# Kernel optimization log

Hardware: AMD Instinct MI355X
Metric: run time of the kernel (lower is better)

Reference implementation:

```python
import jax, jax.numpy as jnp
import numpy as np

N, E, F = 50000, 400000, 128
H0, C0 = 1, 128   # layer 0: heads=1, out=128 (concat=False -> mean over heads)
H1, C1 = 4, 64    # layer 1: heads=4, out=64
EPS_BN = 1e-5
NEG_SLOPE = 0.2


def setup_inputs() -> dict:
    key = jax.random.key(0)
    ks = jax.random.split(key, 12)

    def w(k, shape, fan_in):
        return jax.random.normal(k, shape, jnp.float32) / np.float32(np.sqrt(fan_in))

    return {
        "emb": jax.random.normal(ks[0], (N, F), jnp.float32),
        "edge_weight": jax.random.uniform(ks[1], (E,), jnp.float32),
        # GATv2Conv layer 0 params (lin_l, lin_r, lin_edge, att, out bias)
        "Wl0": w(ks[2], (F, H0 * C0), F), "bl0": jnp.zeros((H0 * C0,), jnp.float32),
        "Wr0": w(ks[3], (F, H0 * C0), F), "br0": jnp.zeros((H0 * C0,), jnp.float32),
        "We0": w(ks[4], (1, H0 * C0), 1), "att0": w(ks[5], (H0, C0), C0),
        "b0": jnp.zeros((C0,), jnp.float32),
        "g0": jnp.ones((C0,), jnp.float32), "be0": jnp.zeros((C0,), jnp.float32),
        # GATv2Conv layer 1 params
        "Wl1": w(ks[6], (C0, H1 * C1), C0), "bl1": jnp.zeros((H1 * C1,), jnp.float32),
        "Wr1": w(ks[7], (C0, H1 * C1), C0), "br1": jnp.zeros((H1 * C1,), jnp.float32),
        "We1": w(ks[8], (1, H1 * C1), 1), "att1": w(ks[9], (H1, C1), C1),
        "b1": jnp.zeros((C1,), jnp.float32),
        "g1": jnp.ones((C1,), jnp.float32), "be1": jnp.zeros((C1,), jnp.float32),
        "edge_index": jax.random.randint(ks[10], (2, E), 0, N, jnp.int32),
    }


def gatv2(x, src, dst, ea, Wl, bl, Wr, br, We, att, b, H, C):
    """PyG GATv2Conv, edge_dim=1, concat=False (mean over heads), eval dropout."""
    n = x.shape[0]
    xl = (x @ Wl + bl).reshape(n, H, C)
    xr = (x @ Wr + br).reshape(n, H, C)
    ef = (ea[:, None] @ We).reshape(-1, H, C)           # [Et,H,C] edge embedding
    m = jax.nn.leaky_relu(xl[src] + xr[dst] + ef, NEG_SLOPE)  # [Et,H,C]
    alpha = jnp.einsum('ehc,hc->eh', m, att)            # attention logits
    amax = jax.ops.segment_max(alpha, dst, num_segments=n)
    ex = jnp.exp(alpha - amax[dst])
    den = jax.ops.segment_sum(ex, dst, num_segments=n)
    a = ex / (den[dst] + 1e-16)                          # segment softmax (PyG eps)
    out = jax.ops.segment_sum(a[:, :, None] * xl[src], dst, num_segments=n)
    return out.mean(axis=1) + b                          # concat=False -> head mean


def batchnorm(x, g, be):
    mu = x.mean(0)
    v = x.var(0)  # biased variance, as torch BN uses for normalization
    return g * (x - mu) * jax.lax.rsqrt(v + EPS_BN) + be


def _forward(emb, edge_weight, Wl0, bl0, Wr0, br0, We0, att0, b0, g0, be0,
             Wl1, bl1, Wr1, br1, We1, att1, b1, g1, be1, edge_index):
    loop = jnp.arange(N, dtype=edge_index.dtype)
    src = jnp.concatenate([edge_index[0], loop])
    dst = jnp.concatenate([edge_index[1], loop])
    # add_self_loops with fill_value='mean' for edge_attr
    ea = jnp.concatenate([edge_weight, jnp.full((N,), edge_weight.mean(), edge_weight.dtype)])
    # NOTE: zip(layer_stack, batchnorm_stack) truncates -> only first 2 of 3 GAT
    # layers execute, each followed by BN + ELU (+ identity dropout, p=0).
    h = gatv2(emb, src, dst, ea, Wl0, bl0, Wr0, br0, We0, att0, b0, H0, C0)
    h = jax.nn.elu(batchnorm(h, g0, be0))
    h = gatv2(h, src, dst, ea, Wl1, bl1, Wr1, br1, We1, att1, b1, H1, C1)
    h = jax.nn.elu(batchnorm(h, g1, be1))
    return h


def reference(emb, edge_weight, Wl0, bl0, Wr0, br0, We0, att0, b0, g0, be0,
              Wl1, bl1, Wr1, br1, We1, att1, b1, g1, be1, edge_index):
    return _forward(emb, edge_weight, Wl0, bl0, Wr0, br0, We0, att0, b0, g0, be0,
                    Wl1, bl1, Wr1, br1, We1, att1, b1, g1, be1, edge_index)
```

## Files before the change

### kernel.cpp

```cpp
#include <hip/hip_runtime.h>
#include <cstdint>
#include <cstddef>
#include <type_traits>

using f32x4 = __attribute__((ext_vector_type(4))) float;
using s16x8 = __attribute__((ext_vector_type(8))) short;

__device__ __forceinline__ ushort f2bf(float x) {
    uint32_t u = __builtin_bit_cast(uint32_t, x);
    u += 0x7fffu + ((u >> 16) & 1u);
    return (ushort)(u >> 16);
}
__device__ __forceinline__ float bflo(uint32_t u) { return __builtin_bit_cast(float, u << 16); }
__device__ __forceinline__ float bfhi(uint32_t u) { return __builtin_bit_cast(float, u & 0xffff0000u); }

__device__ __forceinline__ void dec8(uint4 g, float* x) {
    x[0] = bflo(g.x); x[1] = bfhi(g.x); x[2] = bflo(g.y); x[3] = bfhi(g.y);
    x[4] = bflo(g.z); x[5] = bfhi(g.z); x[6] = bflo(g.w); x[7] = bfhi(g.w);
}

#define GLOAD_LDS16(g, l)                                                                  \
    __builtin_amdgcn_global_load_lds((const __attribute__((address_space(1))) void*)(g),  \
                                     (__attribute__((address_space(3))) void*)(l), 16, 0, 0)

__global__ __launch_bounds__(256) void degree_ew_kernel(const int* __restrict__ ei,
                                                        const float* __restrict__ ew,
                                                        int* __restrict__ deg,
                                                        float* __restrict__ partials,
                                                        int E, int N) {
    __shared__ float red[256];
    int t = threadIdx.x;
    int e = blockIdx.x * 256 + t;
    float s = (e < E) ? ew[e] : 0.f;
    red[t] = s; __syncthreads();
    for (int o = 128; o; o >>= 1) { if (t < o) red[t] += red[t + o]; __syncthreads(); }
    if (t == 0) partials[blockIdx.x] = red[0];
    if (e < E + N) {
        int d = (e < E) ? ei[E + e] : (e - E);
        atomicAdd(&deg[d], 1);
    }
}

__global__ void scan_partial(const int* __restrict__ deg, int n, int* __restrict__ bsum) {
    __shared__ int lds[256];
    int t = threadIdx.x;
    int base = blockIdx.x * 1024 + t * 4;
    int s = 0;
#pragma unroll
    for (int j = 0; j < 4; ++j) if (base + j < n) s += deg[base + j];
    lds[t] = s; __syncthreads();
    for (int o = 128; o; o >>= 1) { if (t < o) lds[t] += lds[t + o]; __syncthreads(); }
    if (t == 0) bsum[blockIdx.x] = lds[0];
}

__global__ void scan_block(const int* __restrict__ bsum, int nb, int* __restrict__ boff,
                           int* __restrict__ row_start, int n, int total,
                           const float* __restrict__ partials, int nbp, int E,
                           float* __restrict__ stats) {
    __shared__ int lds[256];
    __shared__ float fred[256];
    int t = threadIdx.x;
    int v = (t < nb) ? bsum[t] : 0;
    lds[t] = v; __syncthreads();
    for (int o = 1; o < 256; o <<= 1) {
        int y = (t >= o) ? lds[t - o] : 0;
        __syncthreads();
        lds[t] += y;
        __syncthreads();
    }
    if (t < nb) boff[t] = lds[t] - v;
    if (t == 0) row_start[n] = total;
    stats[t] = 0.f; stats[256 + t] = 0.f;
    float fs = 0.f;
    for (int j = t; j < nbp; j += 256) fs += partials[j];
    fred[t] = fs; __syncthreads();
    for (int o = 128; o; o >>= 1) { if (t < o) fred[t] += fred[t + o]; __syncthreads(); }
    if (t == 0) stats[0] = fred[0] / (float)E;
}

__global__ void scan_final(const int* __restrict__ deg, int n, const int* __restrict__ boff,
                           int* __restrict__ row_start) {
    __shared__ int lds[256];
    int t = threadIdx.x;
    int base = blockIdx.x * 1024 + t * 4;
    int d[4], loc[4], s = 0;
#pragma unroll
    for (int j = 0; j < 4; ++j) d[j] = (base + j < n) ? deg[base + j] : 0;
#pragma unroll
    for (int j = 0; j < 4; ++j) { loc[j] = s; s += d[j]; }
    lds[t] = s; __syncthreads();
    for (int o = 1; o < 256; o <<= 1) {
        int y = (t >= o) ? lds[t - o] : 0;
        __syncthreads();
        lds[t] += y;
        __syncthreads();
    }
    int texcl = lds[t] - s + boff[blockIdx.x];
#pragma unroll
    for (int j = 0; j < 4; ++j) if (base + j < n) row_start[base + j] = texcl + loc[j];
}

__global__ void scatter_kernel(const int* __restrict__ ei, const float* __restrict__ ew,
                               const float* __restrict__ ew_mean, const int* __restrict__ row_start,
                               int* __restrict__ cursor, int* __restrict__ csr_src,
                               float* __restrict__ csr_ea, int E, int N) {
    int e = blockIdx.x * blockDim.x + threadIdx.x;
    if (e >= E + N) return;
    int s, d; float w;
    if (e < E) { s = ei[e]; d = ei[E + e]; w = ew[e]; }
    else       { s = d = e - E;            w = ew_mean[0]; }
    int pos = row_start[d] + atomicAdd(&cursor[d], 1);
    csr_src[pos] = s;
    csr_ea[pos] = w;
}

__global__ void prep_kernel(const float* __restrict__ emb, ushort* __restrict__ embb, int n4,
                            const float* __restrict__ Wl0, const float* __restrict__ Wr0,
                            ushort* __restrict__ WT0,
                            const float* __restrict__ Wl1, const float* __restrict__ Wr1,
                            ushort* __restrict__ WT1) {
    int i = blockIdx.x * 256 + threadIdx.x;
    if (i < n4) {
        float4 v = ((const float4*)emb)[i];
        ushort4 o;
        o.x = f2bf(v.x); o.y = f2bf(v.y); o.z = f2bf(v.z); o.w = f2bf(v.w);
        ((ushort4*)embb)[i] = o;
        return;
    }
    int j = i - n4;
    if (j < 128 * 256) {
        int k = j >> 8, c = j & 255;
        float v = (c < 128) ? Wl0[k * 128 + c] : Wr0[k * 128 + (c - 128)];
        WT0[(size_t)c * 128 + k] = f2bf(v);
        return;
    }
    j -= 128 * 256;
    if (j < 128 * 512) {
        int k = j >> 9, c = j & 511;
        float v = (c < 256) ? Wl1[k * 256 + c] : Wr1[k * 256 + (c - 256)];
        WT1[(size_t)c * 128 + k] = f2bf(v);
    }
}

template <bool BN>
__global__ __launch_bounds__(512) void mfma_linear3(const ushort* __restrict__ Xb,
                                                    const ushort* __restrict__ WT,
                                                    const float* __restrict__ bnsums,
                                                    const float* __restrict__ gamma,
                                                    const float* __restrict__ beta,
                                                    const float* __restrict__ bl,
                                                    const float* __restrict__ br,
                                                    ushort* __restrict__ xl,
                                                    ushort* __restrict__ xr,
                                                    int n, int HALF) {
    __shared__ ushort sB[128 * 128];
    __shared__ ushort sA[128 * 128];
    const int tid = threadIdx.x;
    const int c0 = blockIdx.x * 128;
    const int ntiles = (n + 127) >> 7;

    {
        const ushort* src = WT + (size_t)c0 * 128;
#pragma unroll
        for (int it = 0; it < 4; ++it) {
            int f = tid + it * 512;
            int row = f >> 4, ch = f & 15;
            const ushort* g = src + (size_t)row * 128 + ((ch ^ (row & 7)) << 3);
            ushort* lp = sB + (((size_t)it * 512 + (tid & ~63)) << 3);
            GLOAD_LDS16(g, lp);
        }
    }

    const int myc = (tid & 15) * 8;
    const int row0 = tid >> 4;
    const int swc = (tid & 15) ^ (row0 & 7);
    float Af[8], Bf[8];
    if constexpr (BN) {
        float invn = 1.f / (float)n;
#pragma unroll
        for (int j = 0; j < 8; ++j) {
            float mu = bnsums[myc + j] * invn;
            float var = bnsums[128 + myc + j] * invn - mu * mu;
            float rs = rsqrtf(var + 1e-5f);
            Af[j] = gamma[myc + j] * rs;
            Bf[j] = beta[myc + j] - mu * Af[j];
        }
    }

    auto loadA = [&](uint4* r, int rt) {
        int r0 = rt << 7;
#pragma unroll
        for (int it = 0; it < 4; ++it) {
            int gr = r0 + row0 + it * 32; gr = gr < n ? gr : n - 1;
            r[it] = *(const uint4*)&Xb[(size_t)gr * 128 + myc];
        }
    };
    auto writeA = [&](uint4* r) {
#pragma unroll
        for (int it = 0; it < 4; ++it) {
            uint4 o;
            if constexpr (BN) {
                float x[8]; dec8(r[it], x);
                ushort h[8];
#pragma unroll
                for (int j = 0; j < 8; ++j) {
                    float v = fmaf(x[j], Af[j], Bf[j]);
                    v = v > 0.f ? v : __expf(v) - 1.f;
                    h[j] = f2bf(v);
                }
                o.x = h[0] | ((uint32_t)h[1] << 16); o.y = h[2] | ((uint32_t)h[3] << 16);
                o.z = h[4] | ((uint32_t)h[5] << 16); o.w = h[6] | ((uint32_t)h[7] << 16);
            } else {
                o = r[it];
            }
            *(uint4*)&sA[(row0 + it * 32) * 128 + swc * 8] = o;
        }
    };

    const int w = tid >> 6, l = tid & 63, lr = l & 15, lg = l >> 4;
    const bool left = c0 < HALF;
    const float* bias = left ? bl : br;
    ushort* dst = left ? xl : xr;
    const int cb = left ? c0 : c0 - HALF;
    float bv[8];
#pragma unroll
    for (int tn = 0; tn < 8; ++tn) bv[tn] = bias[cb + tn * 16 + lr];
    const int arow = w * 16 + lr;

    int rt = blockIdx.y;
    uint4 rA[4];
    loadA(rA, rt);
    writeA(rA);
    __syncthreads();

    while (true) {
        int nx = rt + gridDim.y;
        if (nx < ntiles) loadA(rA, nx);

        f32x4 acc[8] = {};
#pragma unroll
        for (int kk = 0; kk < 4; ++kk) {
            int ach = (kk * 4 + lg) ^ (arow & 7);
            s16x8 a = *(const s16x8*)&sA[arow * 128 + (ach << 3)];
#pragma unroll
            for (int tn = 0; tn < 8; ++tn) {
                int brow = tn * 16 + lr;
                int bch = (kk * 4 + lg) ^ (brow & 7);
                s16x8 b = *(const s16x8*)&sB[brow * 128 + (bch << 3)];
                acc[tn] = __builtin_amdgcn_mfma_f32_16x16x32_bf16(a, b, acc[tn], 0, 0, 0);
            }
        }
        int rbase = (rt << 7) + w * 16 + lg * 4;
#pragma unroll
        for (int tn = 0; tn < 8; ++tn) {
            int colh = cb + tn * 16 + lr;
#pragma unroll
            for (int r = 0; r < 4; ++r) {
                int row = rbase + r;
                if (row < n) dst[(size_t)row * HALF + colh] = f2bf(acc[tn][r] + bv[tn]);
            }
        }
        if (nx >= ntiles) break;
        __syncthreads();
        writeA(rA);
        __syncthreads();
        rt = nx;
    }
}

template <int H, int C, int LPN>
__global__ __launch_bounds__(256, 8) void gat_agg(const ushort* __restrict__ xl,
                                                  const ushort* __restrict__ xr,
                                                  const int* __restrict__ row_start,
                                                  const int* __restrict__ csr_src,
                                                  const float* __restrict__ csr_ea,
                                                  const float* __restrict__ We,
                                                  const float* __restrict__ att,
                                                  const float* __restrict__ bias,
                                                  ushort* __restrict__ out, int n) {
    constexpr int HC = H * C;
    constexpr int VPL = HC / LPN;
    constexpr int REDW = LPN / H;
    constexpr int NPW = 64 / LPN;
    static_assert(VPL == 8, "");

    const int wid = threadIdx.x >> 6;
    const int lane = threadIdx.x & 63;
    const int sl = lane & (LPN - 1);
    const int sub = lane / LPN;
    const int v = (blockIdx.x * 4 + wid) * NPW + sub;
    const bool valid = v < n;
    const int vv = valid ? v : n - 1;

    const int base = sl * VPL;
    int e = row_start[vv];
    int e1 = valid ? row_start[vv + 1] : e;

    uint4 gN = {}; float wN = 0.f;
    if (e < e1) {
        int s = csr_src[e];
        wN = csr_ea[e];
        gN = *(const uint4*)&xl[(size_t)s * HC + base];
    }

    float xrv[8], wE[8], attv[8];
    dec8(*(const uint4*)&xr[(size_t)vv * HC + base], xrv);
#pragma unroll
    for (int j = 0; j < 8; j += 4) {
        float4 a = *(const float4*)&We[base + j];
        wE[j] = a.x; wE[j + 1] = a.y; wE[j + 2] = a.z; wE[j + 3] = a.w;
        float4 b = *(const float4*)&att[base + j];
        attv[j] = b.x; attv[j + 1] = b.y; attv[j + 2] = b.z; attv[j + 3] = b.w;
    }

    float m = -__builtin_inff(), den = 0.f, acc[8];
#pragma unroll
    for (int j = 0; j < 8; ++j) acc[j] = 0.f;

    for (; e < e1; ++e) {
        uint4 g = gN; float w = wN;
        if (e + 1 < e1) {
            int s = csr_src[e + 1];
            wN = csr_ea[e + 1];
            gN = *(const uint4*)&xl[(size_t)s * HC + base];
        }
        float xf[8];
        dec8(g, xf);
        float t1 = 0.f, t2 = 0.f;
#pragma unroll
        for (int j = 0; j < 8; ++j) {
            float u = xf[j] + fmaf(w, wE[j], xrv[j]);
            t1 = fmaf(u, attv[j], t1);
            t2 = fmaf(__builtin_fabsf(u), attv[j], t2);
        }
        float p = fmaf(0.6f, t1, 0.4f * t2);
#pragma unroll
        for (int o = REDW >> 1; o; o >>= 1) p += __shfl_xor(p, o, 64);
        float d = p - m;
        bool up = d > 0.f;
        float t = __expf(up ? -d : d);
        float sc = up ? t : 1.f;
        float pe = up ? 1.f : t;
        m = up ? p : m;
        den = fmaf(den, sc, pe);
#pragma unroll
        for (int j = 0; j < 8; ++j) acc[j] = fmaf(acc[j], sc, pe * xf[j]);
    }

    float inv = 1.f / (den + 1e-16f);
#pragma unroll
    for (int j = 0; j < 8; ++j) acc[j] *= inv;

    if constexpr (H > 1) {
#pragma unroll
        for (int o = REDW; o < LPN; o <<= 1)
#pragma unroll
            for (int j = 0; j < 8; ++j) acc[j] += __shfl_xor(acc[j], o, 64);
#pragma unroll
        for (int j = 0; j < 8; ++j) acc[j] *= (1.f / (float)H);
    }

    if (valid && sl < C / VPL) {
        float bv[8];
#pragma unroll
        for (int j = 0; j < 8; j += 4) {
            float4 b = *(const float4*)&bias[sl * VPL + j];
            bv[j] = b.x; bv[j + 1] = b.y; bv[j + 2] = b.z; bv[j + 3] = b.w;
        }
        uint4 o;
        o.x = (uint32_t)f2bf(acc[0] + bv[0]) | ((uint32_t)f2bf(acc[1] + bv[1]) << 16);
        o.y = (uint32_t)f2bf(acc[2] + bv[2]) | ((uint32_t)f2bf(acc[3] + bv[3]) << 16);
        o.z = (uint32_t)f2bf(acc[4] + bv[4]) | ((uint32_t)f2bf(acc[5] + bv[5]) << 16);
        o.w = (uint32_t)f2bf(acc[6] + bv[6]) | ((uint32_t)f2bf(acc[7] + bv[7]) << 16);
        *(uint4*)&out[(size_t)v * C + sl * VPL] = o;
    }
}

template <int C>
__global__ __launch_bounds__(256) void bn_stats_bf16(const ushort* __restrict__ x, int n,
                                                     float* __restrict__ sums) {
    constexpr int C2 = C / 2;
    constexpr int RPB = 256 / C2;
    __shared__ float red[256];
    int t = threadIdx.x;
    int c2 = t % C2, rs = t / C2;
    float s0 = 0.f, s1 = 0.f, q0 = 0.f, q1 = 0.f;
    for (int row = blockIdx.x * RPB + rs; row < n; row += gridDim.x * RPB) {
        uint32_t u = *(const uint32_t*)&x[(size_t)row * C + c2 * 2];
        float a = bflo(u), b = bfhi(u);
        s0 += a; q0 += a * a; s1 += b; q1 += b * b;
    }
    float vals[4] = {s0, s1, q0, q1};
    float outv[4];
#pragma unroll
    for (int k = 0; k < 4; ++k) {
        red[t] = vals[k]; __syncthreads();
        if (rs == 0) {
            float s = red[c2];
#pragma unroll
            for (int r = 1; r < RPB; ++r) s += red[c2 + r * C2];
            outv[k] = s;
        }
        __syncthreads();
    }
    if (rs == 0) {
        atomicAdd(&sums[c2 * 2],     outv[0]);
        atomicAdd(&sums[c2 * 2 + 1], outv[1]);
        atomicAdd(&sums[C + c2 * 2],     outv[2]);
        atomicAdd(&sums[C + c2 * 2 + 1], outv[3]);
    }
}

template <int C>
__global__ __launch_bounds__(256) void bn_apply_elu_f32(const ushort* __restrict__ x, int n,
                                                        const float* __restrict__ g,
                                                        const float* __restrict__ be,
                                                        const float* __restrict__ sums,
                                                        float* __restrict__ outf) {
    int total = n * C / 8;
    float invn = 1.f / (float)n;
    for (int i = blockIdx.x * blockDim.x + threadIdx.x; i < total; i += gridDim.x * blockDim.x) {
        uint4 u = ((const uint4*)x)[i];
        int c0 = (i * 8) & (C - 1);
        float r[8] = {bflo(u.x), bfhi(u.x), bflo(u.y), bfhi(u.y),
                      bflo(u.z), bfhi(u.z), bflo(u.w), bfhi(u.w)};
#pragma unroll
        for (int j = 0; j < 8; ++j) {
            int c = c0 + j;
            float mu = sums[c] * invn;
            float var = sums[C + c] * invn - mu * mu;
            float t = g[c] * (r[j] - mu) * rsqrtf(var + 1e-5f) + be[c];
            r[j] = t > 0.f ? t : expm1f(t);
        }
        ((float4*)outf)[i * 2]     = make_float4(r[0], r[1], r[2], r[3]);
        ((float4*)outf)[i * 2 + 1] = make_float4(r[4], r[5], r[6], r[7]);
    }
}

extern "C" void kernel_launch(void* const* d_in, const int* in_sizes, int n_in,
                              void* d_out, int out_size, void* d_ws, size_t ws_size,
                              hipStream_t stream) {
    const float* emb = (const float*)d_in[0];
    const float* ew  = (const float*)d_in[1];
    const float* Wl0 = (const float*)d_in[2];
    const float* bl0 = (const float*)d_in[3];
    const float* Wr0 = (const float*)d_in[4];
    const float* br0 = (const float*)d_in[5];
    const float* We0 = (const float*)d_in[6];
    const float* att0 = (const float*)d_in[7];
    const float* b0  = (const float*)d_in[8];
    const float* g0  = (const float*)d_in[9];
    const float* be0 = (const float*)d_in[10];
    const float* Wl1 = (const float*)d_in[11];
    const float* bl1 = (const float*)d_in[12];
    const float* Wr1 = (const float*)d_in[13];
    const float* br1 = (const float*)d_in[14];
    const float* We1 = (const float*)d_in[15];
    const float* att1 = (const float*)d_in[16];
    const float* b1  = (const float*)d_in[17];
    const float* g1  = (const float*)d_in[18];
    const float* be1 = (const float*)d_in[19];
    const int* ei    = (const int*)d_in[20];

    const int N = in_sizes[0] / 128;
    const int E = in_sizes[1];
    const int Et = E + N;
    float* out = (float*)d_out;

    char* w = (char*)d_ws;
    size_t off = 0;
    auto alloc = [&](size_t bytes) {
        void* p = w + off;
        off = (off + bytes + 255) & ~(size_t)255;
        return p;
    };
    ushort* xlb    = (ushort*)alloc((size_t)N * 256 * 2);
    ushort* xrb    = (ushort*)alloc((size_t)N * 256 * 2);
    ushort* h0b16  = (ushort*)alloc((size_t)N * 128 * 2);
    ushort* out16  = (ushort*)alloc((size_t)N * 64 * 2);
    ushort* embb   = (ushort*)alloc((size_t)N * 128 * 2);
    ushort* WT0    = (ushort*)alloc((size_t)256 * 128 * 2);
    ushort* WT1    = (ushort*)alloc((size_t)512 * 128 * 2);
    int*   deg     = (int*)alloc((size_t)2 * N * 4);
    int*   cursor  = deg + N;
    int*   row_st  = (int*)alloc((size_t)(N + 1) * 4);
    int*   csr_src = (int*)alloc((size_t)Et * 4);
    float* csr_ea  = (float*)alloc((size_t)Et * 4);
    int*   bsum    = (int*)alloc(256 * 4);
    int*   boff    = (int*)alloc(256 * 4);
    float* partials= (float*)alloc(2048 * 4);
    float* stats   = (float*)alloc(512 * 4);
    float* ew_mean = stats;
    float* bn0     = stats + 64;
    float* bn1     = stats + 64 + 256;
    (void)ws_size; (void)n_in; (void)out_size;

    hipMemsetAsync(deg, 0, (size_t)2 * N * 4, stream);

    const int NBE = (Et + 255) / 256;
    degree_ew_kernel<<<NBE, 256, 0, stream>>>(ei, ew, deg, partials, E, N);
    const int NB1 = (N + 1023) / 1024;
    scan_partial<<<NB1, 256, 0, stream>>>(deg, N, bsum);
    scan_block<<<1, 256, 0, stream>>>(bsum, NB1, boff, row_st, N, Et, partials, NBE, E, stats);
    scan_final<<<NB1, 256, 0, stream>>>(deg, N, boff, row_st);
    scatter_kernel<<<NBE, 256, 0, stream>>>(ei, ew, ew_mean, row_st, cursor,
                                            csr_src, csr_ea, E, N);
    const int n4 = N * 128 / 4;
    const int prep_total = n4 + 128 * 256 + 128 * 512;
    prep_kernel<<<(prep_total + 255) / 256, 256, 0, stream>>>(emb, embb, n4,
                                                              Wl0, Wr0, WT0, Wl1, Wr1, WT1);

    const int ntiles = (N + 127) / 128;
    const int GR0 = ntiles < 128 ? ntiles : 128;
    const int GR1 = ntiles < 64 ? ntiles : 64;

    mfma_linear3<false><<<dim3(2, GR0), 512, 0, stream>>>(embb, WT0, nullptr, nullptr, nullptr,
                                                          bl0, br0, xlb, xrb, N, 128);
    gat_agg<1, 128, 16><<<(N + 15) / 16, 256, 0, stream>>>(xlb, xrb, row_st, csr_src, csr_ea,
                                                           We0, att0, b0, h0b16, N);
    bn_stats_bf16<128><<<128, 256, 0, stream>>>(h0b16, N, bn0);

    mfma_linear3<true><<<dim3(4, GR1), 512, 0, stream>>>(h0b16, WT1, bn0, g0, be0,
                                                         bl1, br1, xlb, xrb, N, 256);
    gat_agg<4, 64, 32><<<(N + 7) / 8, 256, 0, stream>>>(xlb, xrb, row_st, csr_src, csr_ea,
                                                        We1, att1, b1, out16, N);
    bn_stats_bf16<64><<<128, 256, 0, stream>>>(out16, N, bn1);
    bn_apply_elu_f32<64><<<1024, 256, 0, stream>>>(out16, N, g1, be1, bn1, out);
}
```

Baseline: 275.0 us.

## Fuse emb bf16 conversion into GEMM, merge weight prep, simplify softmax loop

```diff
diff --git a/kernel.cpp b/kernel.cpp
--- a/kernel.cpp
+++ b/kernel.cpp
@@ -23,21 +23,44 @@
     __builtin_amdgcn_global_load_lds((const __attribute__((address_space(1))) void*)(g),  \
                                      (__attribute__((address_space(3))) void*)(l), 16, 0, 0)
 
-__global__ __launch_bounds__(256) void degree_ew_kernel(const int* __restrict__ ei,
-                                                        const float* __restrict__ ew,
-                                                        int* __restrict__ deg,
-                                                        float* __restrict__ partials,
-                                                        int E, int N) {
+__global__ __launch_bounds__(256) void degree_ew_wt(const int* __restrict__ ei,
+                                                    const float* __restrict__ ew,
+                                                    int* __restrict__ deg,
+                                                    float* __restrict__ partials,
+                                                    int E, int N, int NBE,
+                                                    const float* __restrict__ Wl0,
+                                                    const float* __restrict__ Wr0,
+                                                    ushort* __restrict__ WT0,
+                                                    const float* __restrict__ Wl1,
+                                                    const float* __restrict__ Wr1,
+                                                    ushort* __restrict__ WT1) {
     __shared__ float red[256];
+    int bid = blockIdx.x;
     int t = threadIdx.x;
-    int e = blockIdx.x * 256 + t;
-    float s = (e < E) ? ew[e] : 0.f;
-    red[t] = s; __syncthreads();
-    for (int o = 128; o; o >>= 1) { if (t < o) red[t] += red[t + o]; __syncthreads(); }
-    if (t == 0) partials[blockIdx.x] = red[0];
-    if (e < E + N) {
-        int d = (e < E) ? ei[E + e] : (e - E);
-        atomicAdd(&deg[d], 1);
+    if (bid < NBE) {
+        int e = bid * 256 + t;
+        float s = (e < E) ? ew[e] : 0.f;
+        red[t] = s; __syncthreads();
+        for (int o = 128; o; o >>= 1) { if (t < o) red[t] += red[t + o]; __syncthreads(); }
+        if (t == 0) partials[bid] = red[0];
+        if (e < E + N) {
+            int d = (e < E) ? ei[E + e] : (e - E);
+            atomicAdd(&deg[d], 1);
+        }
+        return;
+    }
+    int j = (bid - NBE) * 256 + t;
+    if (j < 128 * 256) {
+        int k = j >> 8, c = j & 255;
+        float v = (c < 128) ? Wl0[k * 128 + c] : Wr0[k * 128 + (c - 128)];
+        WT0[(size_t)c * 128 + k] = f2bf(v);
+        return;
+    }
+    j -= 128 * 256;
+    if (j < 128 * 512) {
+        int k = j >> 9, c = j & 511;
+        float v = (c < 256) ? Wl1[k * 256 + c] : Wr1[k * 256 + (c - 256)];
+        WT1[(size_t)c * 128 + k] = f2bf(v);
     }
 }
 
@@ -79,7 +102,7 @@
 }
 
 __global__ void scan_final(const int* __restrict__ deg, int n, const int* __restrict__ boff,
-                           int* __restrict__ row_start) {
+                           int* __restrict__ row_start, int* __restrict__ cursor) {
     __shared__ int lds[256];
     int t = threadIdx.x;
     int base = blockIdx.x * 1024 + t * 4;
@@ -97,7 +120,8 @@
     }
     int texcl = lds[t] - s + boff[blockIdx.x];
 #pragma unroll
-    for (int j = 0; j < 4; ++j) if (base + j < n) row_start[base + j] = texcl + loc[j];
+    for (int j = 0; j < 4; ++j)
+        if (base + j < n) { row_start[base + j] = texcl + loc[j]; cursor[base + j] = 0; }
 }
 
 __global__ void scatter_kernel(const int* __restrict__ ei, const float* __restrict__ ew,
@@ -114,36 +138,8 @@
     csr_ea[pos] = w;
 }
 
-__global__ void prep_kernel(const float* __restrict__ emb, ushort* __restrict__ embb, int n4,
-                            const float* __restrict__ Wl0, const float* __restrict__ Wr0,
-                            ushort* __restrict__ WT0,
-                            const float* __restrict__ Wl1, const float* __restrict__ Wr1,
-                            ushort* __restrict__ WT1) {
-    int i = blockIdx.x * 256 + threadIdx.x;
-    if (i < n4) {
-        float4 v = ((const float4*)emb)[i];
-        ushort4 o;
-        o.x = f2bf(v.x); o.y = f2bf(v.y); o.z = f2bf(v.z); o.w = f2bf(v.w);
-        ((ushort4*)embb)[i] = o;
-        return;
-    }
-    int j = i - n4;
-    if (j < 128 * 256) {
-        int k = j >> 8, c = j & 255;
-        float v = (c < 128) ? Wl0[k * 128 + c] : Wr0[k * 128 + (c - 128)];
-        WT0[(size_t)c * 128 + k] = f2bf(v);
-        return;
-    }
-    j -= 128 * 256;
-    if (j < 128 * 512) {
-        int k = j >> 9, c = j & 511;
-        float v = (c < 256) ? Wl1[k * 256 + c] : Wr1[k * 256 + (c - 256)];
-        WT1[(size_t)c * 128 + k] = f2bf(v);
-    }
-}
-
-template <bool BN>
-__global__ __launch_bounds__(512) void mfma_linear3(const ushort* __restrict__ Xb,
+template <int MODE>
+__global__ __launch_bounds__(512) void mfma_linear3(const void* __restrict__ Xv,
                                                     const ushort* __restrict__ WT,
                                                     const float* __restrict__ bnsums,
                                                     const float* __restrict__ gamma,
@@ -153,6 +149,7 @@
                                                     ushort* __restrict__ xl,
                                                     ushort* __restrict__ xr,
                                                     int n, int HALF) {
+    constexpr int LW = (MODE == 1) ? 2 : 1;
     __shared__ ushort sB[128 * 128];
     __shared__ ushort sA[128 * 128];
     const int tid = threadIdx.x;
@@ -175,7 +172,7 @@
     const int row0 = tid >> 4;
     const int swc = (tid & 15) ^ (row0 & 7);
     float Af[8], Bf[8];
-    if constexpr (BN) {
+    if constexpr (MODE == 2) {
         float invn = 1.f / (float)n;
 #pragma unroll
         for (int j = 0; j < 8; ++j) {
@@ -187,20 +184,40 @@
         }
     }
 
-    auto loadA = [&](uint4* r, int rt) {
+    uint4 rA[4][LW];
+    auto loadA = [&](int rt) {
         int r0 = rt << 7;
 #pragma unroll
         for (int it = 0; it < 4; ++it) {
             int gr = r0 + row0 + it * 32; gr = gr < n ? gr : n - 1;
-            r[it] = *(const uint4*)&Xb[(size_t)gr * 128 + myc];
+            if constexpr (MODE == 1) {
+                const float* src = (const float*)Xv + (size_t)gr * 128 + myc;
+                rA[it][0] = *(const uint4*)src;
+                rA[it][1] = *(const uint4*)(src + 4);
+            } else {
+                rA[it][0] = *(const uint4*)((const ushort*)Xv + (size_t)gr * 128 + myc);
+            }
         }
     };
-    auto writeA = [&](uint4* r) {
+    auto writeA = [&]() {
 #pragma unroll
         for (int it = 0; it < 4; ++it) {
             uint4 o;
-            if constexpr (BN) {
-                float x[8]; dec8(r[it], x);
+            if constexpr (MODE == 0) {
+                o = rA[it][0];
+            } else if constexpr (MODE == 1) {
+                float x[8] = {
+                    __builtin_bit_cast(float, rA[it][0].x), __builtin_bit_cast(float, rA[it][0].y),
+                    __builtin_bit_cast(float, rA[it][0].z), __builtin_bit_cast(float, rA[it][0].w),
+                    __builtin_bit_cast(float, rA[it][1].x), __builtin_bit_cast(float, rA[it][1].y),
+                    __builtin_bit_cast(float, rA[it][1].z), __builtin_bit_cast(float, rA[it][1].w)};
+                ushort h[8];
+#pragma unroll
+                for (int j = 0; j < 8; ++j) h[j] = f2bf(x[j]);
+                o.x = h[0] | ((uint32_t)h[1] << 16); o.y = h[2] | ((uint32_t)h[3] << 16);
+                o.z = h[4] | ((uint32_t)h[5] << 16); o.w = h[6] | ((uint32_t)h[7] << 16);
+            } else {
+                float x[8]; dec8(rA[it][0], x);
                 ushort h[8];
 #pragma unroll
                 for (int j = 0; j < 8; ++j) {
@@ -210,8 +227,6 @@
                 }
                 o.x = h[0] | ((uint32_t)h[1] << 16); o.y = h[2] | ((uint32_t)h[3] << 16);
                 o.z = h[4] | ((uint32_t)h[5] << 16); o.w = h[6] | ((uint32_t)h[7] << 16);
-            } else {
-                o = r[it];
             }
             *(uint4*)&sA[(row0 + it * 32) * 128 + swc * 8] = o;
         }
@@ -228,14 +243,13 @@
     const int arow = w * 16 + lr;
 
     int rt = blockIdx.y;
-    uint4 rA[4];
-    loadA(rA, rt);
-    writeA(rA);
+    loadA(rt);
+    writeA();
     __syncthreads();
 
     while (true) {
         int nx = rt + gridDim.y;
-        if (nx < ntiles) loadA(rA, nx);
+        if (nx < ntiles) loadA(nx);
 
         f32x4 acc[8] = {};
 #pragma unroll
@@ -262,7 +276,7 @@
         }
         if (nx >= ntiles) break;
         __syncthreads();
-        writeA(rA);
+        writeA();
         __syncthreads();
         rt = nx;
     }
@@ -293,13 +307,13 @@
     const int vv = valid ? v : n - 1;
 
     const int base = sl * VPL;
-    int e = row_start[vv];
-    int e1 = valid ? row_start[vv + 1] : e;
-
-    uint4 gN = {}; float wN = 0.f;
-    if (e < e1) {
-        int s = csr_src[e];
-        wN = csr_ea[e];
+    const int e0 = row_start[vv];
+    const int e1 = valid ? row_start[vv + 1] : row_start[vv + 1];
+
+    uint4 gN; float wN;
+    {
+        int s = csr_src[e0];
+        wN = csr_ea[e0];
         gN = *(const uint4*)&xl[(size_t)s * HC + base];
     }
 
@@ -313,11 +327,32 @@
         attv[j] = b.x; attv[j + 1] = b.y; attv[j + 2] = b.z; attv[j + 3] = b.w;
     }
 
-    float m = -__builtin_inff(), den = 0.f, acc[8];
-#pragma unroll
-    for (int j = 0; j < 8; ++j) acc[j] = 0.f;
-
-    for (; e < e1; ++e) {
+    float m, den, acc[8];
+    {
+        uint4 g = gN; float w = wN;
+        if (e0 + 1 < e1) {
+            int s = csr_src[e0 + 1];
+            wN = csr_ea[e0 + 1];
+            gN = *(const uint4*)&xl[(size_t)s * HC + base];
+        }
+        float xf[8];
+        dec8(g, xf);
+        float t1 = 0.f, t2 = 0.f;
+#pragma unroll
+        for (int j = 0; j < 8; ++j) {
+            float u = xf[j] + fmaf(w, wE[j], xrv[j]);
+            t1 = fmaf(u, attv[j], t1);
+            t2 = fmaf(__builtin_fabsf(u), attv[j], t2);
+        }
+        float p = fmaf(0.6f, t1, 0.4f * t2);
+#pragma unroll
+        for (int o = REDW >> 1; o; o >>= 1) p += __shfl_xor(p, o, 64);
+        m = p; den = 1.f;
+#pragma unroll
+        for (int j = 0; j < 8; ++j) acc[j] = xf[j];
+    }
+
+    for (int e = e0 + 1; e < e1; ++e) {
         uint4 g = gN; float w = wN;
         if (e + 1 < e1) {
             int s = csr_src[e + 1];
@@ -336,18 +371,22 @@
         float p = fmaf(0.6f, t1, 0.4f * t2);
 #pragma unroll
         for (int o = REDW >> 1; o; o >>= 1) p += __shfl_xor(p, o, 64);
-        float d = p - m;
-        bool up = d > 0.f;
-        float t = __expf(up ? -d : d);
-        float sc = up ? t : 1.f;
-        float pe = up ? 1.f : t;
-        m = up ? p : m;
-        den = fmaf(den, sc, pe);
-#pragma unroll
-        for (int j = 0; j < 8; ++j) acc[j] = fmaf(acc[j], sc, pe * xf[j]);
-    }
-
-    float inv = 1.f / (den + 1e-16f);
+        float dd = p - m;
+        if (__builtin_expect(dd > 8.f, 0)) {
+            float r = __expf(-dd);
+            den = fmaf(den, r, 1.f);
+#pragma unroll
+            for (int j = 0; j < 8; ++j) acc[j] = fmaf(acc[j], r, xf[j]);
+            m = p;
+        } else {
+            float pe = __expf(dd);
+            den += pe;
+#pragma unroll
+            for (int j = 0; j < 8; ++j) acc[j] = fmaf(pe, xf[j], acc[j]);
+        }
+    }
+
+    float inv = 1.f / den;
 #pragma unroll
     for (int j = 0; j < 8; ++j) acc[j] *= inv;
 
@@ -478,7 +517,6 @@
     ushort* xrb    = (ushort*)alloc((size_t)N * 256 * 2);
     ushort* h0b16  = (ushort*)alloc((size_t)N * 128 * 2);
     ushort* out16  = (ushort*)alloc((size_t)N * 64 * 2);
-    ushort* embb   = (ushort*)alloc((size_t)N * 128 * 2);
     ushort* WT0    = (ushort*)alloc((size_t)256 * 128 * 2);
     ushort* WT1    = (ushort*)alloc((size_t)512 * 128 * 2);
     int*   deg     = (int*)alloc((size_t)2 * N * 4);
@@ -495,33 +533,31 @@
     float* bn1     = stats + 64 + 256;
     (void)ws_size; (void)n_in; (void)out_size;
 
-    hipMemsetAsync(deg, 0, (size_t)2 * N * 4, stream);
+    hipMemsetAsync(deg, 0, (size_t)N * 4, stream);
 
     const int NBE = (Et + 255) / 256;
-    degree_ew_kernel<<<NBE, 256, 0, stream>>>(ei, ew, deg, partials, E, N);
+    const int WTB = (128 * 256 + 128 * 512) / 256;
+    degree_ew_wt<<<NBE + WTB, 256, 0, stream>>>(ei, ew, deg, partials, E, N, NBE,
+                                                Wl0, Wr0, WT0, Wl1, Wr1, WT1);
     const int NB1 = (N + 1023) / 1024;
     scan_partial<<<NB1, 256, 0, stream>>>(deg, N, bsum);
     scan_block<<<1, 256, 0, stream>>>(bsum, NB1, boff, row_st, N, Et, partials, NBE, E, stats);
-    scan_final<<<NB1, 256, 0, stream>>>(deg, N, boff, row_st);
+    scan_final<<<NB1, 256, 0, stream>>>(deg, N, boff, row_st, cursor);
     scatter_kernel<<<NBE, 256, 0, stream>>>(ei, ew, ew_mean, row_st, cursor,
                                             csr_src, csr_ea, E, N);
-    const int n4 = N * 128 / 4;
-    const int prep_total = n4 + 128 * 256 + 128 * 512;
-    prep_kernel<<<(prep_total + 255) / 256, 256, 0, stream>>>(emb, embb, n4,
-                                                              Wl0, Wr0, WT0, Wl1, Wr1, WT1);
 
     const int ntiles = (N + 127) / 128;
     const int GR0 = ntiles < 128 ? ntiles : 128;
     const int GR1 = ntiles < 64 ? ntiles : 64;
 
-    mfma_linear3<false><<<dim3(2, GR0), 512, 0, stream>>>(embb, WT0, nullptr, nullptr, nullptr,
-                                                          bl0, br0, xlb, xrb, N, 128);
+    mfma_linear3<1><<<dim3(2, GR0), 512, 0, stream>>>(emb, WT0, nullptr, nullptr, nullptr,
+                                                      bl0, br0, xlb, xrb, N, 128);
     gat_agg<1, 128, 16><<<(N + 15) / 16, 256, 0, stream>>>(xlb, xrb, row_st, csr_src, csr_ea,
                                                            We0, att0, b0, h0b16, N);
     bn_stats_bf16<128><<<128, 256, 0, stream>>>(h0b16, N, bn0);
 
-    mfma_linear3<true><<<dim3(4, GR1), 512, 0, stream>>>(h0b16, WT1, bn0, g0, be0,
-                                                         bl1, br1, xlb, xrb, N, 256);
+    mfma_linear3<2><<<dim3(4, GR1), 512, 0, stream>>>(h0b16, WT1, bn0, g0, be0,
+                                                      bl1, br1, xlb, xrb, N, 256);
     gat_agg<4, 64, 32><<<(N + 7) / 8, 256, 0, stream>>>(xlb, xrb, row_st, csr_src, csr_ea,
                                                         We1, att1, b1, out16, N);
     bn_stats_bf16<64><<<128, 256, 0, stream>>>(out16, N, bn1);
```

Result: faster. 267.7 us (-2.7%).
